# Kernel tuning notes

Measured on AMD Instinct MI355X. Metric: run time of the kernel, lower is better.

## Reference

```python
import jax, jax.numpy as jnp
import numpy as np

N_NODES = 50000
N_EDGES = 500000
D_FEAT = 128


def setup_inputs() -> dict:
    key = jax.random.key(0)
    k1, k2, k3 = jax.random.split(key, 3)
    r = jax.random.normal(k1, (N_NODES, D_FEAT), dtype=jnp.float32)
    e = jax.random.normal(k2, (N_EDGES, D_FEAT), dtype=jnp.float32)
    a = jax.random.randint(k3, (N_EDGES, 2), 0, N_NODES, dtype=jnp.int64)
    return {"r": r, "e": e, "a": a}


def reference(r, e, a):
    # message: gather source/target node features along edges, scale by edge feats
    rij = r[a[:, 0]] * e  # [E, D] messages src -> dst
    rji = r[a[:, 1]] * e  # [E, D] messages dst -> src
    # aggregate: scatter_add into node dimension (fixed num_segments for jit)
    out = jax.ops.segment_sum(rij, a[:, 1], num_segments=r.shape[0])
    out = out + jax.ops.segment_sum(rji, a[:, 0], num_segments=r.shape[0])
    return out  # [N, D]
```

## Files before the change

kernel.cpp:

```cpp
#include <hip/hip_runtime.h>
#include <hip/hip_fp16.h>


#define D_FEAT 128
#define SCAN_TILE 1024
#define CHUNK 4096

__global__ __launch_bounds__(256) void hist1_kernel(
    const int* __restrict__ a, unsigned* __restrict__ ghist,
    int n_entries, int nwords) {
    extern __shared__ unsigned h[];
    for (int i = threadIdx.x; i < nwords; i += blockDim.x) h[i] = 0u;
    __syncthreads();
    int s = blockIdx.x * CHUNK;
    int e = s + CHUNK;
    if (e > n_entries) e = n_entries;
    for (int idx = s + threadIdx.x; idx < e; idx += blockDim.x) {
        int n = a[idx];
        atomicAdd(&h[n >> 2], 1u << ((n & 3) * 8));
    }
    __syncthreads();
    unsigned* dst = ghist + (size_t)blockIdx.x * nwords;
    for (int i = threadIdx.x; i < nwords; i += blockDim.x) dst[i] = h[i];
}

__global__ void merge2_kernel(const unsigned* __restrict__ ghist,
                              unsigned char* __restrict__ base,
                              int* __restrict__ deg,
                              int n_nodes, int nblk, int nwords) {
    int n = blockIdx.x * blockDim.x + threadIdx.x;
    if (n >= n_nodes) return;
    int w = n >> 2, sh = (n & 3) * 8;
    int run = 0;
    for (int b = 0; b < nblk; ++b) {
        base[(size_t)b * n_nodes + n] = (unsigned char)run;
        run += (int)((ghist[(size_t)b * nwords + w] >> sh) & 0xffu);
    }
    deg[n] = run;
}

__global__ void scanA_kernel(const int* __restrict__ deg, int* __restrict__ bsum,
                             int n) {
    __shared__ int wsum[16];
    int t = threadIdx.x, lane = t & 63, w = t >> 6;
    int i = blockIdx.x * SCAN_TILE + t;
    int v = (i < n) ? deg[i] : 0;
    #pragma unroll
    for (int off = 32; off > 0; off >>= 1) v += __shfl_down(v, off, 64);
    if (lane == 0) wsum[w] = v;
    __syncthreads();
    if (t == 0) {
        int s = 0;
        #pragma unroll
        for (int k = 0; k < 16; ++k) s += wsum[k];
        bsum[blockIdx.x] = s;
    }
}

__global__ void scanB_kernel(int* __restrict__ bsum, int* __restrict__ bbase,
                             int* __restrict__ offs, int nblk, int n) {
    if (threadIdx.x == 0) {
        int run = 0;
        for (int b = 0; b < nblk; ++b) {
            bbase[b] = run;
            run += bsum[b];
        }
        offs[n] = run;
    }
}

__global__ void scanC_kernel(const int* __restrict__ deg, int* __restrict__ offs,
                             const int* __restrict__ bbase, int n) {
    __shared__ int wsum[16];
    int t = threadIdx.x, lane = t & 63, w = t >> 6;
    int i = blockIdx.x * SCAN_TILE + t;
    int v = (i < n) ? deg[i] : 0;
    int x = v;
    #pragma unroll
    for (int off = 1; off < 64; off <<= 1) {
        int y = __shfl_up(x, off, 64);
        if (lane >= off) x += y;
    }
    if (lane == 63) wsum[w] = x;
    __syncthreads();
    if (w == 0 && lane < 16) {
        int s = wsum[lane];
        #pragma unroll
        for (int off = 1; off < 16; off <<= 1) {
            int y = __shfl_up(s, off, 64);
            if (lane >= off) s += y;
        }
        wsum[lane] = s;
    }
    __syncthreads();
    int wbase = (w == 0) ? 0 : wsum[w - 1];
    if (i < n) offs[i] = x - v + wbase + bbase[blockIdx.x];
}

__global__ __launch_bounds__(256) void fill3_kernel(
    const int* __restrict__ a, const int* __restrict__ offs,
    const unsigned char* __restrict__ base, int2* __restrict__ pl,
    int n_entries, int n_nodes, int nwords) {
    extern __shared__ unsigned cur[];
    for (int i = threadIdx.x; i < nwords; i += blockDim.x) cur[i] = 0u;
    __syncthreads();
    int s = blockIdx.x * CHUNK;
    int e = s + CHUNK;
    if (e > n_entries) e = n_entries;
    const unsigned char* brow = base + (size_t)blockIdx.x * n_nodes;
    for (int idx = s + threadIdx.x; idx < e; idx += blockDim.x) {
        int other  = a[idx];
        int center = a[idx ^ 1];
        int sh = (center & 3) * 8;
        unsigned old = atomicAdd(&cur[center >> 2], 1u << sh);
        int local = (int)((old >> sh) & 0xffu);
        int pos = offs[center] + (int)brow[center] + local;
        pl[pos] = make_int2(idx >> 1, other);
    }
}

__global__ __launch_bounds__(256) void gather_f32_kernel(
    const float* __restrict__ r, const float* __restrict__ e,
    const int* __restrict__ offs, const int2* __restrict__ pl,
    float* __restrict__ out, int n_nodes) {
    int n = blockIdx.x * 4 + (threadIdx.x >> 6);
    if (n >= n_nodes) return;
    int lane = threadIdx.x & 63;
    int start = offs[n];
    int end = offs[n + 1];
    float accx = 0.f, accy = 0.f;
    int i = start;
    for (; i + 4 <= end; i += 4) {
        int2 p0 = pl[i];
        int2 p1 = pl[i + 1];
        int2 p2 = pl[i + 2];
        int2 p3 = pl[i + 3];
        float2 e0 = *((const float2*)(e + (size_t)p0.x * D_FEAT) + lane);
        float2 r0 = *((const float2*)(r + (size_t)p0.y * D_FEAT) + lane);
        float2 e1 = *((const float2*)(e + (size_t)p1.x * D_FEAT) + lane);
        float2 r1 = *((const float2*)(r + (size_t)p1.y * D_FEAT) + lane);
        float2 e2 = *((const float2*)(e + (size_t)p2.x * D_FEAT) + lane);
        float2 r2 = *((const float2*)(r + (size_t)p2.y * D_FEAT) + lane);
        float2 e3 = *((const float2*)(e + (size_t)p3.x * D_FEAT) + lane);
        float2 r3 = *((const float2*)(r + (size_t)p3.y * D_FEAT) + lane);
        accx += e0.x * r0.x; accy += e0.y * r0.y;
        accx += e1.x * r1.x; accy += e1.y * r1.y;
        accx += e2.x * r2.x; accy += e2.y * r2.y;
        accx += e3.x * r3.x; accy += e3.y * r3.y;
    }
    for (; i < end; ++i) {
        int2 p0 = pl[i];
        float2 e0 = *((const float2*)(e + (size_t)p0.x * D_FEAT) + lane);
        float2 r0 = *((const float2*)(r + (size_t)p0.y * D_FEAT) + lane);
        accx += e0.x * r0.x; accy += e0.y * r0.y;
    }
    float2 res;
    res.x = accx;
    res.y = accy;
    *((float2*)(out + (size_t)n * D_FEAT) + lane) = res;
}


__global__ void hist_kernel(const int* __restrict__ a, int* __restrict__ deg,
                            int n_elems) {
    int i = blockIdx.x * blockDim.x + threadIdx.x;
    if (i < n_elems) atomicAdd(&deg[a[i]], 1);
}

__global__ void fill_kernel(const int* __restrict__ a, int* __restrict__ cursor,
                            int2* __restrict__ pl, int n_entries) {
    int k = blockIdx.x * blockDim.x + threadIdx.x;
    if (k >= n_entries) return;
    int edge = k >> 1, j = k & 1;
    int other  = a[2 * edge + j];
    int center = a[2 * edge + (j ^ 1)];
    int pos = atomicAdd(&cursor[center], 1);
    pl[pos] = make_int2(edge, other);
}

__global__ void scanC_cursor_kernel(int* __restrict__ deg, int* __restrict__ offs,
                                    const int* __restrict__ bbase, int n) {
    __shared__ int wsum[16];
    int t = threadIdx.x, lane = t & 63, w = t >> 6;
    int i = blockIdx.x * SCAN_TILE + t;
    int v = (i < n) ? deg[i] : 0;
    int x = v;
    #pragma unroll
    for (int off = 1; off < 64; off <<= 1) {
        int y = __shfl_up(x, off, 64);
        if (lane >= off) x += y;
    }
    if (lane == 63) wsum[w] = x;
    __syncthreads();
    if (w == 0 && lane < 16) {
        int s = wsum[lane];
        #pragma unroll
        for (int off = 1; off < 16; off <<= 1) {
            int y = __shfl_up(s, off, 64);
            if (lane >= off) s += y;
        }
        wsum[lane] = s;
    }
    __syncthreads();
    int wbase = (w == 0) ? 0 : wsum[w - 1];
    if (i < n) {
        int excl = x - v + wbase + bbase[blockIdx.x];
        offs[i] = excl;
        deg[i] = excl;
    }
}

__global__ void mp_scatter_kernel(const float* __restrict__ r,
                                  const float* __restrict__ e,
                                  const int* __restrict__ a,
                                  float* __restrict__ out,
                                  int n_edges) {
    long long gid = (long long)blockIdx.x * blockDim.x + threadIdx.x;
    int edge = (int)(gid >> 7);
    int feat = (int)(gid & 127);
    if (edge >= n_edges) return;
    int s = a[2 * edge];
    int d = a[2 * edge + 1];
    float ev = e[(long long)edge * D_FEAT + feat];
    float rs = r[(long long)s * D_FEAT + feat];
    float rd = r[(long long)d * D_FEAT + feat];
    atomicAdd(&out[(long long)d * D_FEAT + feat], rs * ev);
    atomicAdd(&out[(long long)s * D_FEAT + feat], rd * ev);
}

extern "C" void kernel_launch(void* const* d_in, const int* in_sizes, int n_in,
                              void* d_out, int out_size, void* d_ws, size_t ws_size,
                              hipStream_t stream) {
    const float* r = (const float*)d_in[0];
    const float* e = (const float*)d_in[1];
    const int*   a = (const int*)d_in[2];
    float* out = (float*)d_out;
    (void)n_in;
    (void)out_size;

    int n_nodes   = in_sizes[0] / D_FEAT;
    int n_edges   = in_sizes[1] / D_FEAT;
    int n_entries = 2 * n_edges;

    int block = 256;
    int grid_e = (n_entries + block - 1) / block;
    int nblk_scan = (n_nodes + SCAN_TILE - 1) / SCAN_TILE;
    int nblk_c = (n_entries + CHUNK - 1) / CHUNK;
    int nwords = (n_nodes + 3) / 4;
    size_t lds_bytes = (size_t)nwords * sizeof(unsigned);

    {
        size_t ghist_words = (size_t)nblk_c * nwords;
        size_t base_bytes  = (((size_t)nblk_c * n_nodes) + 3) & ~(size_t)3;
        size_t ints_tail   = (size_t)n_nodes + (size_t)(n_nodes + 1)
                           + 2 * (size_t)nblk_scan;
        size_t head_bytes  = ghist_words * 4 + base_bytes + ints_tail * 4;
        head_bytes = (head_bytes + 7) & ~(size_t)7;
        size_t need = head_bytes + (size_t)n_entries * sizeof(int2);
        if (ws_size >= need && nblk_scan <= 1024 && lds_bytes <= 64 * 1024) {
            unsigned*      ghist = (unsigned*)d_ws;
            unsigned char* basep = (unsigned char*)(ghist + ghist_words);
            int*           deg   = (int*)(basep + base_bytes);
            int*           offs  = deg + n_nodes;
            int*           bsum  = offs + n_nodes + 1;
            int*           bbase = bsum + nblk_scan;
            int2*          pl    = (int2*)((char*)d_ws + head_bytes);

            hist1_kernel<<<nblk_c, block, lds_bytes, stream>>>(a, ghist,
                                                               n_entries,
                                                               nwords);
            int grid_m = (n_nodes + block - 1) / block;
            merge2_kernel<<<grid_m, block, 0, stream>>>(ghist, basep, deg,
                                                        n_nodes, nblk_c,
                                                        nwords);
            scanA_kernel<<<nblk_scan, SCAN_TILE, 0, stream>>>(deg, bsum,
                                                              n_nodes);
            scanB_kernel<<<1, 64, 0, stream>>>(bsum, bbase, offs, nblk_scan,
                                               n_nodes);
            scanC_kernel<<<nblk_scan, SCAN_TILE, 0, stream>>>(deg, offs, bbase,
                                                              n_nodes);
            fill3_kernel<<<nblk_c, block, lds_bytes, stream>>>(a, offs, basep,
                                                               pl, n_entries,
                                                               n_nodes, nwords);
            int grid_g = (n_nodes + 3) / 4;
            gather_f32_kernel<<<grid_g, 256, 0, stream>>>(r, e, offs, pl, out,
                                                          n_nodes);
            return;
        }
    }

    {
        size_t ints_head = (size_t)n_nodes + (size_t)(n_nodes + 1)
                         + 2 * (size_t)nblk_scan;
        ints_head = (ints_head + 1) & ~(size_t)1;
        size_t need = ints_head * sizeof(int) + (size_t)n_entries * sizeof(int2);
        if (ws_size >= need && nblk_scan <= 1024) {
            int*  deg  = (int*)d_ws;
            int*  offs = deg + n_nodes;
            int*  bsum = offs + n_nodes + 1;
            int*  bbase= bsum + nblk_scan;
            int2* pl   = (int2*)((int*)d_ws + ints_head);

            hipMemsetAsync(deg, 0, (size_t)n_nodes * sizeof(int), stream);
            hist_kernel<<<grid_e, block, 0, stream>>>(a, deg, n_entries);
            scanA_kernel<<<nblk_scan, SCAN_TILE, 0, stream>>>(deg, bsum, n_nodes);
            scanB_kernel<<<1, 64, 0, stream>>>(bsum, bbase, offs, nblk_scan,
                                               n_nodes);
            scanC_cursor_kernel<<<nblk_scan, SCAN_TILE, 0, stream>>>(deg, offs,
                                                                     bbase,
                                                                     n_nodes);
            fill_kernel<<<grid_e, block, 0, stream>>>(a, deg, pl, n_entries);
            int grid_g = (n_nodes + 3) / 4;
            gather_f32_kernel<<<grid_g, 256, 0, stream>>>(r, e, offs, pl, out,
                                                          n_nodes);
            return;
        }
    }

    hipMemsetAsync(d_out, 0, (size_t)out_size * sizeof(float), stream);
    long long total = (long long)n_edges * D_FEAT;
    long long grid = (total + block - 1) / block;
    mp_scatter_kernel<<<(int)grid, block, 0, stream>>>(r, e, a, out, n_edges);
}
```

Before: 539.8 us.

## Gather from fp16 node copy, split merge into two stages, use nontemporal loads

The histogram kernel now also converts r to a packed fp16 copy, and the gather reads that copy, halving node-feature gather traffic. The sequential per-node prefix over all chunk blocks is split into eight parallel groups plus a second pass, which shortens the serial merge loop. Edge features and the pair list are read with nontemporal loads. The fp16 copy of r loses precision, which may exceed the reference tolerance. The workspace also grows.

```diff
diff --git a/kernel.cpp b/kernel.cpp
--- a/kernel.cpp
+++ b/kernel.cpp
@@ -5,10 +5,25 @@
 #define D_FEAT 128
 #define SCAN_TILE 1024
 #define CHUNK 4096
+#define G_GRP 8
+
+typedef float vf2 __attribute__((ext_vector_type(2)));
+
+__device__ inline unsigned pack_h2(float a, float b) {
+    __half2 h;
+    h.x = __float2half_rn(a);
+    h.y = __float2half_rn(b);
+    return *reinterpret_cast<unsigned*>(&h);
+}
+__device__ inline float2 unpack_h2(unsigned u) {
+    __half2 h = *reinterpret_cast<__half2*>(&u);
+    return __half22float2(h);
+}
 
 __global__ __launch_bounds__(256) void hist1_kernel(
-    const int* __restrict__ a, unsigned* __restrict__ ghist,
-    int n_entries, int nwords) {
+    const int* __restrict__ a, const float* __restrict__ r,
+    unsigned* __restrict__ ghist, uint2* __restrict__ r16,
+    int n_entries, int nwords, int n_r4) {
     extern __shared__ unsigned h[];
     for (int i = threadIdx.x; i < nwords; i += blockDim.x) h[i] = 0u;
     __syncthreads();
@@ -22,19 +37,46 @@
     __syncthreads();
     unsigned* dst = ghist + (size_t)blockIdx.x * nwords;
     for (int i = threadIdx.x; i < nwords; i += blockDim.x) dst[i] = h[i];
-}
-
-__global__ void merge2_kernel(const unsigned* __restrict__ ghist,
-                              unsigned char* __restrict__ base,
-                              int* __restrict__ deg,
-                              int n_nodes, int nblk, int nwords) {
+    int tid = blockIdx.x * blockDim.x + threadIdx.x;
+    int nth = gridDim.x * blockDim.x;
+    for (int i = tid; i < n_r4; i += nth) {
+        const float4 v = ((const float4*)r)[i];
+        uint2 p;
+        p.x = pack_h2(v.x, v.y);
+        p.y = pack_h2(v.z, v.w);
+        r16[i] = p;
+    }
+}
+
+__global__ void m2a_kernel(const unsigned* __restrict__ ghist,
+                           unsigned char* __restrict__ base,
+                           unsigned char* __restrict__ gsum,
+                           int n_nodes, int nblk, int gblk, int nwords) {
     int n = blockIdx.x * blockDim.x + threadIdx.x;
     if (n >= n_nodes) return;
+    int g = blockIdx.y;
+    int b0 = g * gblk;
+    int b1 = b0 + gblk;
+    if (b1 > nblk) b1 = nblk;
     int w = n >> 2, sh = (n & 3) * 8;
     int run = 0;
-    for (int b = 0; b < nblk; ++b) {
+    for (int b = b0; b < b1; ++b) {
         base[(size_t)b * n_nodes + n] = (unsigned char)run;
         run += (int)((ghist[(size_t)b * nwords + w] >> sh) & 0xffu);
+    }
+    gsum[(size_t)g * n_nodes + n] = (unsigned char)run;
+}
+
+__global__ void m2b_kernel(const unsigned char* __restrict__ gsum,
+                           unsigned char* __restrict__ gbase,
+                           int* __restrict__ deg, int n_nodes) {
+    int n = blockIdx.x * blockDim.x + threadIdx.x;
+    if (n >= n_nodes) return;
+    int run = 0;
+    #pragma unroll
+    for (int g = 0; g < G_GRP; ++g) {
+        gbase[(size_t)g * n_nodes + n] = (unsigned char)run;
+        run += (int)gsum[(size_t)g * n_nodes + n];
     }
     deg[n] = run;
 }
@@ -99,8 +141,9 @@
 
 __global__ __launch_bounds__(256) void fill3_kernel(
     const int* __restrict__ a, const int* __restrict__ offs,
-    const unsigned char* __restrict__ base, int2* __restrict__ pl,
-    int n_entries, int n_nodes, int nwords) {
+    const unsigned char* __restrict__ base,
+    const unsigned char* __restrict__ gbase, int2* __restrict__ pl,
+    int n_entries, int n_nodes, int nwords, int gblk) {
     extern __shared__ unsigned cur[];
     for (int i = threadIdx.x; i < nwords; i += blockDim.x) cur[i] = 0u;
     __syncthreads();
@@ -108,19 +151,20 @@
     int e = s + CHUNK;
     if (e > n_entries) e = n_entries;
     const unsigned char* brow = base + (size_t)blockIdx.x * n_nodes;
+    const unsigned char* grow = gbase + (size_t)(blockIdx.x / gblk) * n_nodes;
     for (int idx = s + threadIdx.x; idx < e; idx += blockDim.x) {
         int other  = a[idx];
         int center = a[idx ^ 1];
         int sh = (center & 3) * 8;
         unsigned old = atomicAdd(&cur[center >> 2], 1u << sh);
         int local = (int)((old >> sh) & 0xffu);
-        int pos = offs[center] + (int)brow[center] + local;
+        int pos = offs[center] + (int)grow[center] + (int)brow[center] + local;
         pl[pos] = make_int2(idx >> 1, other);
     }
 }
 
-__global__ __launch_bounds__(256) void gather_f32_kernel(
-    const float* __restrict__ r, const float* __restrict__ e,
+__global__ __launch_bounds__(256) void gather_nt_kernel(
+    const unsigned* __restrict__ r16, const float* __restrict__ e,
     const int* __restrict__ offs, const int2* __restrict__ pl,
     float* __restrict__ out, int n_nodes) {
     int n = blockIdx.x * 4 + (threadIdx.x >> 6);
@@ -131,28 +175,43 @@
     float accx = 0.f, accy = 0.f;
     int i = start;
     for (; i + 4 <= end; i += 4) {
-        int2 p0 = pl[i];
-        int2 p1 = pl[i + 1];
-        int2 p2 = pl[i + 2];
-        int2 p3 = pl[i + 3];
-        float2 e0 = *((const float2*)(e + (size_t)p0.x * D_FEAT) + lane);
-        float2 r0 = *((const float2*)(r + (size_t)p0.y * D_FEAT) + lane);
-        float2 e1 = *((const float2*)(e + (size_t)p1.x * D_FEAT) + lane);
-        float2 r1 = *((const float2*)(r + (size_t)p1.y * D_FEAT) + lane);
-        float2 e2 = *((const float2*)(e + (size_t)p2.x * D_FEAT) + lane);
-        float2 r2 = *((const float2*)(r + (size_t)p2.y * D_FEAT) + lane);
-        float2 e3 = *((const float2*)(e + (size_t)p3.x * D_FEAT) + lane);
-        float2 r3 = *((const float2*)(r + (size_t)p3.y * D_FEAT) + lane);
-        accx += e0.x * r0.x; accy += e0.y * r0.y;
-        accx += e1.x * r1.x; accy += e1.y * r1.y;
-        accx += e2.x * r2.x; accy += e2.y * r2.y;
-        accx += e3.x * r3.x; accy += e3.y * r3.y;
+        unsigned long long w0 = __builtin_nontemporal_load(
+            (const unsigned long long*)(pl + i));
+        unsigned long long w1 = __builtin_nontemporal_load(
+            (const unsigned long long*)(pl + i + 1));
+        unsigned long long w2 = __builtin_nontemporal_load(
+            (const unsigned long long*)(pl + i + 2));
+        unsigned long long w3 = __builtin_nontemporal_load(
+            (const unsigned long long*)(pl + i + 3));
+        int e0i = (int)(unsigned)w0, o0 = (int)(w0 >> 32);
+        int e1i = (int)(unsigned)w1, o1 = (int)(w1 >> 32);
+        int e2i = (int)(unsigned)w2, o2 = (int)(w2 >> 32);
+        int e3i = (int)(unsigned)w3, o3 = (int)(w3 >> 32);
+        vf2 ev0 = __builtin_nontemporal_load(
+            ((const vf2*)(e + (size_t)e0i * D_FEAT)) + lane);
+        vf2 ev1 = __builtin_nontemporal_load(
+            ((const vf2*)(e + (size_t)e1i * D_FEAT)) + lane);
+        vf2 ev2 = __builtin_nontemporal_load(
+            ((const vf2*)(e + (size_t)e2i * D_FEAT)) + lane);
+        vf2 ev3 = __builtin_nontemporal_load(
+            ((const vf2*)(e + (size_t)e3i * D_FEAT)) + lane);
+        float2 r0 = unpack_h2(r16[(size_t)o0 * 64 + lane]);
+        float2 r1 = unpack_h2(r16[(size_t)o1 * 64 + lane]);
+        float2 r2 = unpack_h2(r16[(size_t)o2 * 64 + lane]);
+        float2 r3 = unpack_h2(r16[(size_t)o3 * 64 + lane]);
+        accx += ev0.x * r0.x; accy += ev0.y * r0.y;
+        accx += ev1.x * r1.x; accy += ev1.y * r1.y;
+        accx += ev2.x * r2.x; accy += ev2.y * r2.y;
+        accx += ev3.x * r3.x; accy += ev3.y * r3.y;
     }
     for (; i < end; ++i) {
-        int2 p0 = pl[i];
-        float2 e0 = *((const float2*)(e + (size_t)p0.x * D_FEAT) + lane);
-        float2 r0 = *((const float2*)(r + (size_t)p0.y * D_FEAT) + lane);
-        accx += e0.x * r0.x; accy += e0.y * r0.y;
+        unsigned long long w0 = __builtin_nontemporal_load(
+            (const unsigned long long*)(pl + i));
+        int e0i = (int)(unsigned)w0, o0 = (int)(w0 >> 32);
+        vf2 ev0 = __builtin_nontemporal_load(
+            ((const vf2*)(e + (size_t)e0i * D_FEAT)) + lane);
+        float2 r0 = unpack_h2(r16[(size_t)o0 * 64 + lane]);
+        accx += ev0.x * r0.x; accy += ev0.y * r0.y;
     }
     float2 res;
     res.x = accx;
@@ -208,6 +267,29 @@
         offs[i] = excl;
         deg[i] = excl;
     }
+}
+
+__global__ __launch_bounds__(256) void gather_f32_kernel(
+    const float* __restrict__ r, const float* __restrict__ e,
+    const int* __restrict__ offs, const int2* __restrict__ pl,
+    float* __restrict__ out, int n_nodes) {
+    int n = blockIdx.x * 4 + (threadIdx.x >> 6);
+    if (n >= n_nodes) return;
+    int lane = threadIdx.x & 63;
+    int start = offs[n];
+    int end = offs[n + 1];
+    float accx = 0.f, accy = 0.f;
+    for (int i = start; i < end; ++i) {
+        int2 p0 = pl[i];
+        float2 ev0 = *((const float2*)(e + (size_t)p0.x * D_FEAT) + lane);
+        float2 rv0 = *((const float2*)(r + (size_t)p0.y * D_FEAT) + lane);
+        accx += ev0.x * rv0.x;
+        accy += ev0.y * rv0.y;
+    }
+    float2 res;
+    res.x = accx;
+    res.y = accy;
+    *((float2*)(out + (size_t)n * D_FEAT) + lane) = res;
 }
 
 __global__ void mp_scatter_kernel(const float* __restrict__ r,
@@ -236,55 +318,61 @@
     const int*   a = (const int*)d_in[2];
     float* out = (float*)d_out;
     (void)n_in;
-    (void)out_size;
 
     int n_nodes   = in_sizes[0] / D_FEAT;
     int n_edges   = in_sizes[1] / D_FEAT;
     int n_entries = 2 * n_edges;
+    int n_r4      = in_sizes[0] / 4;
 
     int block = 256;
     int grid_e = (n_entries + block - 1) / block;
     int nblk_scan = (n_nodes + SCAN_TILE - 1) / SCAN_TILE;
     int nblk_c = (n_entries + CHUNK - 1) / CHUNK;
+    int gblk   = (nblk_c + G_GRP - 1) / G_GRP;
     int nwords = (n_nodes + 3) / 4;
     size_t lds_bytes = (size_t)nwords * sizeof(unsigned);
 
     {
         size_t ghist_words = (size_t)nblk_c * nwords;
         size_t base_bytes  = (((size_t)nblk_c * n_nodes) + 3) & ~(size_t)3;
+        size_t gsum_bytes  = (((size_t)G_GRP * n_nodes) + 3) & ~(size_t)3;
         size_t ints_tail   = (size_t)n_nodes + (size_t)(n_nodes + 1)
                            + 2 * (size_t)nblk_scan;
-        size_t head_bytes  = ghist_words * 4 + base_bytes + ints_tail * 4;
+        size_t head_bytes  = ghist_words * 4 + base_bytes + 2 * gsum_bytes
+                           + (size_t)n_r4 * sizeof(uint2) + ints_tail * 4;
         head_bytes = (head_bytes + 7) & ~(size_t)7;
         size_t need = head_bytes + (size_t)n_entries * sizeof(int2);
         if (ws_size >= need && nblk_scan <= 1024 && lds_bytes <= 64 * 1024) {
             unsigned*      ghist = (unsigned*)d_ws;
             unsigned char* basep = (unsigned char*)(ghist + ghist_words);
-            int*           deg   = (int*)(basep + base_bytes);
+            unsigned char* gsum  = basep + base_bytes;
+            unsigned char* gbase = gsum + gsum_bytes;
+            uint2*         r16   = (uint2*)(gbase + gsum_bytes);
+            int*           deg   = (int*)(r16 + n_r4);
             int*           offs  = deg + n_nodes;
             int*           bsum  = offs + n_nodes + 1;
             int*           bbase = bsum + nblk_scan;
             int2*          pl    = (int2*)((char*)d_ws + head_bytes);
 
-            hist1_kernel<<<nblk_c, block, lds_bytes, stream>>>(a, ghist,
-                                                               n_entries,
-                                                               nwords);
+            hist1_kernel<<<nblk_c, block, lds_bytes, stream>>>(
+                a, r, ghist, r16, n_entries, nwords, n_r4);
+            dim3 gm2a((n_nodes + block - 1) / block, G_GRP);
+            m2a_kernel<<<gm2a, block, 0, stream>>>(ghist, basep, gsum,
+                                                   n_nodes, nblk_c, gblk,
+                                                   nwords);
             int grid_m = (n_nodes + block - 1) / block;
-            merge2_kernel<<<grid_m, block, 0, stream>>>(ghist, basep, deg,
-                                                        n_nodes, nblk_c,
-                                                        nwords);
+            m2b_kernel<<<grid_m, block, 0, stream>>>(gsum, gbase, deg, n_nodes);
             scanA_kernel<<<nblk_scan, SCAN_TILE, 0, stream>>>(deg, bsum,
                                                               n_nodes);
             scanB_kernel<<<1, 64, 0, stream>>>(bsum, bbase, offs, nblk_scan,
                                                n_nodes);
             scanC_kernel<<<nblk_scan, SCAN_TILE, 0, stream>>>(deg, offs, bbase,
                                                               n_nodes);
-            fill3_kernel<<<nblk_c, block, lds_bytes, stream>>>(a, offs, basep,
-                                                               pl, n_entries,
-                                                               n_nodes, nwords);
+            fill3_kernel<<<nblk_c, block, lds_bytes, stream>>>(
+                a, offs, basep, gbase, pl, n_entries, n_nodes, nwords, gblk);
             int grid_g = (n_nodes + 3) / 4;
-            gather_f32_kernel<<<grid_g, 256, 0, stream>>>(r, e, offs, pl, out,
-                                                          n_nodes);
+            gather_nt_kernel<<<grid_g, 256, 0, stream>>>(
+                (const unsigned*)r16, e, offs, pl, out, n_nodes);
             return;
         }
     }
```

New measurement: 499.4 us. -7.5%, faster.
